# Optimization experiments

Hardware: AMD Instinct MI355X
Metric: run time of the kernel (lower is better)

Reference implementation:

```python
import jax, jax.numpy as jnp
import numpy as np

WIDTH = 768
HEAD = 64

def setup_inputs() -> dict:
    key = jax.random.key(0)
    ks = jax.random.split(key, 8)
    x = jax.random.normal(ks[0], (8, 2048, WIDTH), dtype=jnp.float32)
    mask = jax.random.randint(ks[1], (2048, 2048), 0, 2, dtype=jnp.int32)
    s = 1.0 / np.sqrt(WIDTH)
    Wq = jax.random.normal(ks[2], (WIDTH, HEAD), dtype=jnp.float32) * s
    Wk = jax.random.normal(ks[3], (WIDTH, HEAD), dtype=jnp.float32) * s
    Wv = jax.random.normal(ks[4], (WIDTH, HEAD), dtype=jnp.float32) * s
    bq = jax.random.normal(ks[5], (HEAD,), dtype=jnp.float32) * 0.01
    bk = jax.random.normal(ks[6], (HEAD,), dtype=jnp.float32) * 0.01
    bv = jax.random.normal(ks[7], (HEAD,), dtype=jnp.float32) * 0.01
    return {"x": x, "Wq": Wq, "bq": bq, "Wk": Wk, "bk": bk, "Wv": Wv, "bv": bv, "mask": mask}

def reference(x, Wq, bq, Wk, bk, Wv, bv, mask) -> jnp.ndarray:
    # x: [B, N, width]; projections -> [B, N, head]
    Q = jnp.einsum('bnw,wh->bnh', x, Wq) + bq
    K = jnp.einsum('bnw,wh->bnh', x, Wk) + bk
    V = jnp.einsum('bnw,wh->bnh', x, Wv) + bv
    scale = 1.0 / jnp.sqrt(jnp.asarray(Q.shape[-1], dtype=Q.dtype))
    scores = jnp.einsum('bqh,bkh->bqk', Q, K) * scale  # [B, N, N]
    scores = jnp.where(mask == 0, -jnp.inf, scores)
    attn = jax.nn.softmax(scores, axis=-1)
    return jnp.einsum('bqk,bkh->bqh', attn, V)
```

## Files before the change

### kernel.cpp

```cpp
#include <hip/hip_runtime.h>

typedef short  s8v   __attribute__((ext_vector_type(8)));
typedef float  f32x4 __attribute__((ext_vector_type(4)));

#define SEQ 2048
#define WID 768

__device__ __forceinline__ unsigned fbits(float f) {
    union { float f; unsigned u; } v; v.f = f; return v.u;
}
__device__ __forceinline__ float bitsf(unsigned u) {
    union { unsigned u; float f; } v; v.u = u; return v.f;
}
__device__ __forceinline__ unsigned short f2b(float f) {
    unsigned u = fbits(f);
    return (unsigned short)((u + 0x7FFFu + ((u >> 16) & 1u)) >> 16);
}
__device__ __forceinline__ unsigned packRNE(float a, float b) {
    unsigned ta = fbits(a) + 0x7FFFu + ((fbits(a) >> 16) & 1u);
    unsigned tb = fbits(b) + 0x7FFFu + ((fbits(b) >> 16) & 1u);
    return __builtin_amdgcn_perm(tb, ta, 0x07060302u);
}
__device__ __forceinline__ unsigned packTRUNC(float a, float b) {
    return __builtin_amdgcn_perm(fbits(b), fbits(a), 0x07060302u);
}
__device__ __forceinline__ f32x4 zero4() { f32x4 z = {0.f, 0.f, 0.f, 0.f}; return z; }

__device__ __forceinline__ void async16(const unsigned short* g, void* l) {
    __builtin_amdgcn_global_load_lds(
        (const __attribute__((address_space(1))) unsigned int*)g,
        (__attribute__((address_space(3))) unsigned int*)l, 16, 0, 0);
}
__device__ __forceinline__ void async16f(const float* g, void* l) {
    __builtin_amdgcn_global_load_lds(
        (const __attribute__((address_space(1))) unsigned int*)g,
        (__attribute__((address_space(3))) unsigned int*)l, 16, 0, 0);
}

__global__ __launch_bounds__(256) void convert_w_kernel(
    const float* __restrict__ Wq, const float* __restrict__ Wk, const float* __restrict__ Wv,
    unsigned short* __restrict__ WF)
{
    const int s2 = blockIdx.x * 256 + threadIdx.x;
    const int chunk = s2 >> 6, l = s2 & 63;
    const int ntg = chunk / 24, r = chunk - ntg * 24;
    const int kc = r >> 1, h = r & 1;
    const int mat = ntg >> 2;
    const int col = (ntg & 3) * 16 + (l & 15);
    const int k0 = kc * 64 + h * 32 + (l >> 4) * 8;
    const float* Wm = (mat == 0) ? Wq : (mat == 1) ? Wk : Wv;
    float p[8];
    #pragma unroll
    for (int j = 0; j < 8; ++j) p[j] = Wm[(size_t)(k0 + j) * 64 + col];
    uint4 w;
    w.x = packRNE(p[0], p[1]); w.y = packRNE(p[2], p[3]);
    w.z = packRNE(p[4], p[5]); w.w = packRNE(p[6], p[7]);
    *(uint4*)&WF[(size_t)s2 * 8] = w;
}

__global__ __launch_bounds__(256, 4) void qkv_proj_kernel(
    const float* __restrict__ x, const unsigned short* __restrict__ WF,
    const float* __restrict__ bq, const float* __restrict__ bk, const float* __restrict__ bv,
    unsigned short* __restrict__ QF, unsigned short* __restrict__ KF,
    unsigned short* __restrict__ VF)
{
    __shared__ __align__(16) unsigned char SM[32768];
    unsigned short (*St)[200] = (unsigned short(*)[200])SM;

    const int tid = threadIdx.x;
    const int wv = tid >> 6, lane = tid & 63, quad = lane >> 4, c = lane & 15;
    const int cg = wv;
    const int rowb = blockIdx.x * 32;

    float bias[3];
    #pragma unroll
    for (int nt = 0; nt < 3; ++nt) {
        int col = cg * 48 + nt * 16 + c;
        const float* B = (col < 64) ? bq : (col < 128) ? bk : bv;
        bias[nt] = B[col & 63];
    }

    auto issue = [&](int kc, int b) {
        unsigned char* base = SM + b * 16384;
        #pragma unroll
        for (int r = 0; r < 4; ++r) {
            const int t = wv * 4 + r;
            if (t < 4) {
                const int mt = t >> 1, jh = t & 1;
                const float* src = x + (size_t)(rowb + mt * 16 + c) * WID
                                     + kc * 32 + quad * 8 + jh * 4;
                async16f(src, base + (mt * 2 + jh) * 1024);
            } else {
                const int i = t - 4;
                const unsigned short* src =
                    WF + (((size_t)i * 12 + (kc >> 1)) * 2 + (kc & 1)) * 512 + lane * 8;
                async16(src, base + 4096 + i * 1024);
            }
        }
    };

    f32x4 acc[2][3];
    #pragma unroll
    for (int mt = 0; mt < 2; ++mt)
        #pragma unroll
        for (int nt = 0; nt < 3; ++nt) acc[mt][nt] = zero4();

    issue(0, 0);
    for (int kc = 0; kc < 24; ++kc) {
        const int b = kc & 1;
        __syncthreads();
        if (kc < 23) issue(kc + 1, b ^ 1);

        const unsigned char* base = SM + b * 16384;
        s8v af[2];
        #pragma unroll
        for (int mt = 0; mt < 2; ++mt) {
            float4 f0 = *(const float4*)(base + (mt * 2 + 0) * 1024 + lane * 16);
            float4 f1 = *(const float4*)(base + (mt * 2 + 1) * 1024 + lane * 16);
            union { uint4 u; s8v v; } a;
            a.u.x = packRNE(f0.x, f0.y);
            a.u.y = packRNE(f0.z, f0.w);
            a.u.z = packRNE(f1.x, f1.y);
            a.u.w = packRNE(f1.z, f1.w);
            af[mt] = a.v;
        }
        s8v bf[3];
        #pragma unroll
        for (int nt = 0; nt < 3; ++nt)
            bf[nt] = *(const s8v*)(base + 4096 + (cg * 3 + nt) * 1024 + lane * 16);
        #pragma unroll
        for (int mt = 0; mt < 2; ++mt)
            #pragma unroll
            for (int nt = 0; nt < 3; ++nt)
                acc[mt][nt] = __builtin_amdgcn_mfma_f32_16x16x32_bf16(
                    af[mt], bf[nt], acc[mt][nt], 0, 0, 0);
    }

    __syncthreads();
    #pragma unroll
    for (int mt = 0; mt < 2; ++mt)
        #pragma unroll
        for (int nt = 0; nt < 3; ++nt)
            #pragma unroll
            for (int i = 0; i < 4; ++i)
                St[mt * 16 + quad * 4 + i][cg * 48 + nt * 16 + c]
                    = f2b(acc[mt][nt][i] + bias[nt]);
    __syncthreads();

    const int kb  = rowb >> 6;
    const int q0k = (rowb & 63) >> 2;
    const int ks0 = (rowb & 63) >> 5;

    {
        const int g = tid >> 7, ks = (tid >> 6) & 1, l = tid & 63;
        uint4 v = *(uint4*)&St[g * 16 + (l & 15)][ks * 32 + (l >> 4) * 8];
        *(uint4*)&QF[(((size_t)(rowb >> 4) + g) * 2 + ks) * 512 + (size_t)l * 8] = v;
    }
    {
        const int ksnt = tid >> 5, e = tid & 31;
        const int ks = ksnt >> 2, nt = ksnt & 3;
        const int qd = e >> 3, cc = e & 7;
        uint4 v = *(uint4*)&St[4 * cc + nt][64 + ks * 32 + qd * 8];
        *(uint4*)&KF[(((size_t)kb * 8 + ksnt) * 64 + qd * 16 + q0k + cc) * 8] = v;
    }
    {
        const int nt = tid >> 6, qd = (tid >> 4) & 3, cc = tid & 15;
        unsigned short p[8];
        #pragma unroll
        for (int s = 0; s < 8; ++s) p[s] = St[qd * 8 + s][128 + nt * 16 + cc];
        uint4 w;
        w.x = (unsigned)p[0] | ((unsigned)p[1] << 16);
        w.y = (unsigned)p[2] | ((unsigned)p[3] << 16);
        w.z = (unsigned)p[4] | ((unsigned)p[5] << 16);
        w.w = (unsigned)p[6] | ((unsigned)p[7] << 16);
        *(uint4*)&VF[(((size_t)kb * 8 + ks0 * 4 + nt) * 64 + qd * 16 + cc) * 8] = w;
    }
}

__global__ __launch_bounds__(512, 4) void attn_kernel(
    const unsigned short* __restrict__ QF, const unsigned short* __restrict__ KF,
    const unsigned short* __restrict__ VF, const int* __restrict__ mask,
    float* __restrict__ out)
{
    __shared__ unsigned short Ks[4][4096];
    __shared__ __align__(16) unsigned char PsOb[17408];
    __shared__ float Lbuf[32];
    unsigned short (*Ps)[16][68] = (unsigned short(*)[16][68])PsOb;
    float (*Obuf)[68]            = (float(*)[68])PsOb;

    const int tid = threadIdx.x;
    const int wv = tid >> 6, lane = tid & 63, quad = lane >> 4, c = lane & 15;
    const int sl = wv & 3, qh = wv >> 2;
    const int blk = blockIdx.x;
    const int bb = blk & 7, qt = blk >> 3;
    const int qrow_blk = qt * 32;

    s8v qf[2];
    {
        const size_t qgrp = (size_t)bb * 128 + qt * 2 + qh;
        #pragma unroll
        for (int ks = 0; ks < 2; ++ks)
            qf[ks] = *(const s8v*)&QF[(qgrp * 2 + ks) * 512 + (size_t)lane * 8];
    }

    f32x4 O[4];
    float lro[4];
    #pragma unroll
    for (int nt = 0; nt < 4; ++nt) O[nt] = zero4();
    #pragma unroll
    for (int i = 0; i < 4; ++i) lro[i] = 0.f;

    auto k_dma = [&](int kt) {
        const size_t kbg = (size_t)bb * 32 + sl * 8 + kt;
        #pragma unroll
        for (int r = 0; r < 4; ++r) {
            const int ch = qh * 4 + r;
            async16(KF + (kbg * 8 + ch) * 512 + lane * 8, &Ks[sl][ch * 512]);
        }
    };

    k_dma(0);
    for (int kt = 0; kt < 8; ++kt) {
        const int kb64 = sl * 8 + kt;
        const size_t kbg = (size_t)bb * 32 + kb64;

        int4 mrow[4];
        #pragma unroll
        for (int i = 0; i < 4; ++i) {
            const int q = qrow_blk + qh * 16 + quad * 4 + i;
            mrow[i] = *(const int4*)&mask[(size_t)q * SEQ + kb64 * 64 + 4 * c];
        }

        __syncthreads();

        f32x4 S[4];
        #pragma unroll
        for (int nt = 0; nt < 4; ++nt) S[nt] = zero4();
        #pragma unroll
        for (int ks = 0; ks < 2; ++ks) {
            s8v kfr[4];
            #pragma unroll
            for (int nt = 0; nt < 4; ++nt)
                kfr[nt] = *(const s8v*)&Ks[sl][((ks * 4 + nt) * 64 + lane) * 8];
            #pragma unroll
            for (int nt = 0; nt < 4; ++nt)
                S[nt] = __builtin_amdgcn_mfma_f32_16x16x32_bf16(qf[ks], kfr[nt], S[nt], 0, 0, 0);
        }

        s8v vf[8];
        #pragma unroll
        for (int ch = 0; ch < 8; ++ch)
            vf[ch] = *(const s8v*)&VF[(kbg * 8 + ch) * 512 + (size_t)lane * 8];

        #pragma unroll
        for (int i = 0; i < 4; ++i) {
            float p4[4];
            #pragma unroll
            for (int nt = 0; nt < 4; ++nt) {
                float e = exp2f(fmaf(S[nt][i], 0.18033688011112042f, -21.640425613334451f));
                const int mb = (nt == 0) ? mrow[i].x : (nt == 1) ? mrow[i].y
                             : (nt == 2) ? mrow[i].z : mrow[i].w;
                p4[nt] = mb ? e : 0.f;
            }
            unsigned u0 = packTRUNC(p4[0], p4[1]);
            unsigned u1 = packTRUNC(p4[2], p4[3]);
            lro[i] += bitsf(u0 << 16) + bitsf(u0 & 0xFFFF0000u)
                    + bitsf(u1 << 16) + bitsf(u1 & 0xFFFF0000u);
            *(uint2*)&Ps[wv][quad * 4 + i][4 * c] = make_uint2(u0, u1);
        }

        #pragma unroll
        for (int ks = 0; ks < 2; ++ks) {
            s8v a = *(const s8v*)&Ps[wv][c][ks * 32 + quad * 8];
            #pragma unroll
            for (int nt = 0; nt < 4; ++nt)
                O[nt] = __builtin_amdgcn_mfma_f32_16x16x32_bf16(a, vf[ks * 4 + nt], O[nt], 0, 0, 0);
        }

        __syncthreads();
        if (kt < 7) k_dma(kt + 1);
    }

    __syncthreads();
    #pragma unroll
    for (int j = 0; j < 5; ++j) {
        int idx = tid + 512 * j;
        if (idx < 32 * 68) ((float*)Obuf)[idx] = 0.f;
    }
    if (tid < 32) Lbuf[tid] = 0.f;
    __syncthreads();
    #pragma unroll
    for (int i = 0; i < 4; ++i) {
        float l = lro[i];
        l += __shfl_xor(l, 1);
        l += __shfl_xor(l, 2);
        l += __shfl_xor(l, 4);
        l += __shfl_xor(l, 8);
        if (c == 0) atomicAdd(&Lbuf[qh * 16 + quad * 4 + i], l);
        #pragma unroll
        for (int nt = 0; nt < 4; ++nt)
            atomicAdd(&Obuf[qh * 16 + quad * 4 + i][nt * 16 + c], O[nt][i]);
    }
    __syncthreads();
    {
        const int r = tid >> 4, d4 = (tid & 15) * 4;
        const float invL = 1.0f / Lbuf[r];
        float4 v = *(float4*)&Obuf[r][d4];
        float4 o = make_float4(v.x * invL, v.y * invL, v.z * invL, v.w * invL);
        *(float4*)&out[((size_t)bb * SEQ + qrow_blk + r) * 64 + d4] = o;
    }
}

extern "C" void kernel_launch(void* const* d_in, const int* in_sizes, int n_in,
                              void* d_out, int out_size, void* d_ws, size_t ws_size,
                              hipStream_t stream)
{
    const float* x    = (const float*)d_in[0];
    const float* Wq   = (const float*)d_in[1];
    const float* bq   = (const float*)d_in[2];
    const float* Wk   = (const float*)d_in[3];
    const float* bk   = (const float*)d_in[4];
    const float* Wv   = (const float*)d_in[5];
    const float* bv   = (const float*)d_in[6];
    const int*   mask = (const int*)d_in[7];
    float* out = (float*)d_out;

    unsigned short* QF = (unsigned short*)d_ws;
    unsigned short* KF = QF + (size_t)16384 * 64;
    unsigned short* VF = KF + (size_t)16384 * 64;
    unsigned short* WF = VF + (size_t)16384 * 64;

    convert_w_kernel<<<72, 256, 0, stream>>>(Wq, Wk, Wv, WF);
    qkv_proj_kernel<<<512, 256, 0, stream>>>(x, WF, bq, bk, bv, QF, KF, VF);
    attn_kernel<<<512, 512, 0, stream>>>(QF, KF, VF, mask, out);
}
```

Baseline: 190.7 us.

## Pre-pack the int32 mask into per-lane bitmasks and stream them via LDS DMA

Adds a preprocessing kernel that packs the int32 attention mask into 32-bit words laid out per MFMA lane, one word per lane for each 32x64 tile. The attention kernel then fetches these words asynchronously into shared memory alongside the K tiles, so it no longer re-reads the full int32 mask once per batch (eight times over). V fragment loads are also split and moved next to the PV MFMAs to lower register pressure. The cost is an extra kernel launch and one pass over the full mask per call, and the later V loads may expose more global-load latency.

```diff
diff --git a/kernel.cpp b/kernel.cpp
--- a/kernel.cpp
+++ b/kernel.cpp
@@ -35,6 +35,33 @@
     __builtin_amdgcn_global_load_lds(
         (const __attribute__((address_space(1))) unsigned int*)g,
         (__attribute__((address_space(3))) unsigned int*)l, 16, 0, 0);
+}
+__device__ __forceinline__ void async4(const unsigned* g, void* l) {
+    __builtin_amdgcn_global_load_lds(
+        (const __attribute__((address_space(1))) unsigned int*)g,
+        (__attribute__((address_space(3))) unsigned int*)l, 4, 0, 0);
+}
+
+__global__ __launch_bounds__(256) void convert_mask_kernel(
+    const int* __restrict__ mask, unsigned* __restrict__ PM)
+{
+    const int tid = threadIdx.x;
+    const int gid  = blockIdx.x * 4 + (tid >> 6);
+    const int lane = tid & 63, quad = lane >> 4, c = lane & 15;
+    const int qb = gid >> 5, kb = gid & 31;
+    unsigned w = 0;
+    #pragma unroll
+    for (int mt = 0; mt < 2; ++mt)
+        #pragma unroll
+        for (int i = 0; i < 4; ++i) {
+            const int q = qb * 32 + mt * 16 + quad * 4 + i;
+            const int4 mm = *(const int4*)&mask[(size_t)q * SEQ + kb * 64 + 4 * c];
+            if (mm.x) w |= 1u << (mt * 16 + i * 4 + 0);
+            if (mm.y) w |= 1u << (mt * 16 + i * 4 + 1);
+            if (mm.z) w |= 1u << (mt * 16 + i * 4 + 2);
+            if (mm.w) w |= 1u << (mt * 16 + i * 4 + 3);
+        }
+    PM[(size_t)gid * 64 + lane] = w;
 }
 
 __global__ __launch_bounds__(256) void convert_w_kernel(
@@ -179,10 +206,11 @@
 
 __global__ __launch_bounds__(512, 4) void attn_kernel(
     const unsigned short* __restrict__ QF, const unsigned short* __restrict__ KF,
-    const unsigned short* __restrict__ VF, const int* __restrict__ mask,
+    const unsigned short* __restrict__ VF, const unsigned* __restrict__ PM,
     float* __restrict__ out)
 {
     __shared__ unsigned short Ks[4][4096];
+    __shared__ unsigned PMs[4][64];
     __shared__ __align__(16) unsigned char PsOb[17408];
     __shared__ float Lbuf[32];
     unsigned short (*Ps)[16][68] = (unsigned short(*)[16][68])PsOb;
@@ -217,19 +245,13 @@
             const int ch = qh * 4 + r;
             async16(KF + (kbg * 8 + ch) * 512 + lane * 8, &Ks[sl][ch * 512]);
         }
+        if (qh == 0)
+            async4(PM + ((size_t)qt * 32 + sl * 8 + kt) * 64 + lane, &PMs[sl][0]);
     };
 
     k_dma(0);
     for (int kt = 0; kt < 8; ++kt) {
-        const int kb64 = sl * 8 + kt;
-        const size_t kbg = (size_t)bb * 32 + kb64;
-
-        int4 mrow[4];
-        #pragma unroll
-        for (int i = 0; i < 4; ++i) {
-            const int q = qrow_blk + qh * 16 + quad * 4 + i;
-            mrow[i] = *(const int4*)&mask[(size_t)q * SEQ + kb64 * 64 + 4 * c];
-        }
+        const size_t kbg = (size_t)bb * 32 + sl * 8 + kt;
 
         __syncthreads();
 
@@ -247,20 +269,14 @@
                 S[nt] = __builtin_amdgcn_mfma_f32_16x16x32_bf16(qf[ks], kfr[nt], S[nt], 0, 0, 0);
         }
 
-        s8v vf[8];
-        #pragma unroll
-        for (int ch = 0; ch < 8; ++ch)
-            vf[ch] = *(const s8v*)&VF[(kbg * 8 + ch) * 512 + (size_t)lane * 8];
-
+        const unsigned pmh = PMs[sl][lane] >> (qh * 16);
         #pragma unroll
         for (int i = 0; i < 4; ++i) {
             float p4[4];
             #pragma unroll
             for (int nt = 0; nt < 4; ++nt) {
                 float e = exp2f(fmaf(S[nt][i], 0.18033688011112042f, -21.640425613334451f));
-                const int mb = (nt == 0) ? mrow[i].x : (nt == 1) ? mrow[i].y
-                             : (nt == 2) ? mrow[i].z : mrow[i].w;
-                p4[nt] = mb ? e : 0.f;
+                p4[nt] = ((pmh >> (i * 4 + nt)) & 1u) ? e : 0.f;
             }
             unsigned u0 = packTRUNC(p4[0], p4[1]);
             unsigned u1 = packTRUNC(p4[2], p4[3]);
@@ -271,10 +287,14 @@
 
         #pragma unroll
         for (int ks = 0; ks < 2; ++ks) {
+            s8v vf4[4];
+            #pragma unroll
+            for (int nt = 0; nt < 4; ++nt)
+                vf4[nt] = *(const s8v*)&VF[(kbg * 8 + ks * 4 + nt) * 512 + (size_t)lane * 8];
             s8v a = *(const s8v*)&Ps[wv][c][ks * 32 + quad * 8];
             #pragma unroll
             for (int nt = 0; nt < 4; ++nt)
-                O[nt] = __builtin_amdgcn_mfma_f32_16x16x32_bf16(a, vf[ks * 4 + nt], O[nt], 0, 0, 0);
+                O[nt] = __builtin_amdgcn_mfma_f32_16x16x32_bf16(a, vf4[nt], O[nt], 0, 0, 0);
         }
 
         __syncthreads();
@@ -329,8 +349,10 @@
     unsigned short* KF = QF + (size_t)16384 * 64;
     unsigned short* VF = KF + (size_t)16384 * 64;
     unsigned short* WF = VF + (size_t)16384 * 64;
-
+    unsigned*       PM = (unsigned*)(WF + (size_t)192 * WID);
+
+    convert_mask_kernel<<<512, 256, 0, stream>>>(mask, PM);
     convert_w_kernel<<<72, 256, 0, stream>>>(Wq, Wk, Wv, WF);
     qkv_proj_kernel<<<512, 256, 0, stream>>>(x, WF, bq, bk, bv, QF, KF, VF);
-    attn_kernel<<<512, 512, 0, stream>>>(QF, KF, VF, mask, out);
-}
+    attn_kernel<<<512, 512, 0, stream>>>(QF, KF, VF, PM, out);
+}
```

New measurement: 174.0 us. 8.8% less time.
